# Kernel tuning notes

Measured on AMD Instinct MI355X. Metric: run time of the kernel, lower is better.

## Reference

```python
import jax, jax.numpy as jnp
import numpy as np

N_NODES = 100000
N_EDGES = 6400000
IN_CH, HID, OUT_CH = 14, 16, 8


def setup_inputs() -> dict:
    key = jax.random.key(0)
    ks = jax.random.split(key, 10)
    x = jax.random.normal(ks[0], (N_NODES, IN_CH), dtype=jnp.float32)
    edge_index = jax.random.randint(ks[1], (2, N_EDGES), 0, N_NODES, dtype=jnp.int64)
    edge_attr = jax.random.normal(ks[2], (N_EDGES, 4), dtype=jnp.float32)
    # SAGEConv params: lin_l (neighbor aggr, with bias), lin_r (root, no bias)
    def glorot(k, shape):
        fan_in = shape[1]
        return jax.random.normal(k, shape, dtype=jnp.float32) / jnp.sqrt(jnp.float32(fan_in))
    W1_l = glorot(ks[3], (HID, IN_CH)); b1 = jnp.zeros((HID,), jnp.float32)
    W1_r = glorot(ks[4], (HID, IN_CH))
    W2_l = glorot(ks[5], (OUT_CH, HID)); b2 = jnp.zeros((OUT_CH,), jnp.float32)
    W2_r = glorot(ks[6], (OUT_CH, HID))
    return {"x": x, "edge_index": edge_index, "edge_attr": edge_attr,
            "W1_l": W1_l, "b1": b1, "W1_r": W1_r,
            "W2_l": W2_l, "b2": b2, "W2_r": W2_r}


def sage_conv(x, src, dst, W_l, b_l, W_r):
    # mean aggregation of neighbor features at destination nodes
    msg = x[src]                                            # [E, F]
    s = jax.ops.segment_sum(msg, dst, num_segments=N_NODES)  # [N, F]
    cnt = jax.ops.segment_sum(jnp.ones((src.shape[0],), x.dtype), dst,
                              num_segments=N_NODES)
    mean = s / jnp.maximum(cnt, 1.0)[:, None]
    # out = lin_l(mean) + lin_r(x)
    return mean @ W_l.T + b_l + x @ W_r.T


def reference(x, edge_index, edge_attr, W1_l, b1, W1_r, W2_l, b2, W2_r):
    src, dst = edge_index[0], edge_index[1]
    h = jax.nn.relu(sage_conv(x, src, dst, W1_l, b1, W1_r))
    # F.dropout(training=self.training) -> identity in eval mode
    out = sage_conv(h, src, dst, W2_l, b2, W2_r)
    return out
```

## Files before the change

kernel.cpp:

```cpp
#include <hip/hip_runtime.h>

#define N_NODES 100000
#define N_EDGES 6400000
#define IN_CH 14
#define HID 16
#define OUT_CH 8

#define NBINS 1024
#define BINW 98
#define NCLS 8
#define SLABC 1152
#define BINREG (NCLS * SLABC)
#define BINBUF_WORDS (NBINS * BINREG)
#define SORT_CAP 7168
#define BF_THREADS 1024
#define BF_TILE 8192
#define BF_EPT (BF_TILE / BF_THREADS)
#define N_TILES ((N_EDGES + BF_TILE - 1) / BF_TILE)
#define LHN 128

__device__ __forceinline__ unsigned short f2bf(float f) {
    unsigned u = __float_as_uint(f);
    u += 0x7fffu + ((u >> 16) & 1u);
    return (unsigned short)(u >> 16);
}

__global__ void prep_kernel(const float* __restrict__ x, unsigned short* __restrict__ xb,
                            int* __restrict__ tail) {
    int i = blockIdx.x * blockDim.x + threadIdx.x;
    if (i < NCLS * NBINS) tail[i] = 0;
    if (i >= (NBINS * BINW) * 16) return;
    int n = i >> 4, c = i & 15;
    float v = (n < N_NODES && c < IN_CH) ? x[n * IN_CH + c] : 0.0f;
    xb[i] = f2bf(v);
}

__global__ __launch_bounds__(BF_THREADS)
void binfill_kernel(const uint4* __restrict__ src4, const uint4* __restrict__ dst4,
                    int* __restrict__ tail, unsigned* __restrict__ binbuf) {
    __shared__ unsigned stile[BF_TILE];
    __shared__ unsigned short stbin[BF_TILE];
    __shared__ int lh[NBINS];
    __shared__ int lx[NBINS];
    __shared__ int lofs[NBINS];
    __shared__ int wsum[16];

    const int t = threadIdx.x;
    const int lane = t & 63;
    const int wv = t >> 6;
    const int cls = blockIdx.x & (NCLS - 1);
    const long long tb = (long long)blockIdx.x * BF_TILE;

    lh[t] = 0;
    __syncthreads();

    unsigned epack[BF_EPT];
    int      ebin[BF_EPT];
    int      erank[BF_EPT];

#pragma unroll
    for (int sw = 0; sw < BF_EPT / 4; ++sw) {
        long long u = tb / 4 + (long long)sw * BF_THREADS + t;
        int k = sw * 4;
        if (u * 4 < N_EDGES) {
            uint4 s = src4[u];
            uint4 d = dst4[u];
            unsigned b;
            b = d.x / BINW; epack[k+0] = s.x | ((d.x - b*BINW) << 17); ebin[k+0] = (int)b; erank[k+0] = atomicAdd(&lh[b], 1);
            b = d.y / BINW; epack[k+1] = s.y | ((d.y - b*BINW) << 17); ebin[k+1] = (int)b; erank[k+1] = atomicAdd(&lh[b], 1);
            b = d.z / BINW; epack[k+2] = s.z | ((d.z - b*BINW) << 17); ebin[k+2] = (int)b; erank[k+2] = atomicAdd(&lh[b], 1);
            b = d.w / BINW; epack[k+3] = s.w | ((d.w - b*BINW) << 17); ebin[k+3] = (int)b; erank[k+3] = atomicAdd(&lh[b], 1);
        } else {
            ebin[k+0] = ebin[k+1] = ebin[k+2] = ebin[k+3] = -1;
        }
    }
    __syncthreads();

    int v = lh[t];
    int incl = v;
#pragma unroll
    for (int d = 1; d < 64; d <<= 1) {
        int o = __shfl_up(incl, d, 64);
        if (lane >= d) incl += o;
    }
    if (lane == 63) wsum[wv] = incl;
    __syncthreads();
    if (t < 16) {
        int s = wsum[t];
        int si = s;
#pragma unroll
        for (int d = 1; d < 16; d <<= 1) {
            int o = __shfl_up(si, d, 16);
            if (t >= d) si += o;
        }
        wsum[t] = si - s;
    }
    __syncthreads();
    lx[t] = incl - v + wsum[wv];
    lofs[t] = atomicAdd(&tail[cls * NBINS + t], v);
    __syncthreads();

#pragma unroll
    for (int k = 0; k < BF_EPT; ++k) {
        if (ebin[k] >= 0) {
            int pos = lx[ebin[k]] + erank[k];
            stile[pos] = epack[k];
            stbin[pos] = (unsigned short)ebin[k];
        }
    }
    __syncthreads();

    int cnt = (int)((N_EDGES - tb < BF_TILE) ? (N_EDGES - tb) : BF_TILE);
    for (int i = t; i < cnt; i += BF_THREADS) {
        int b = stbin[i];
        int slot = lofs[b] + (i - lx[b]);
        if ((unsigned)slot < (unsigned)SLABC)
            binbuf[b * BINREG + cls * SLABC + slot] = stile[i];
    }
}

__global__ __launch_bounds__(512)
void sortagg1_kernel(const unsigned* __restrict__ xb, const float* __restrict__ x,
                     unsigned* __restrict__ binbuf, const int* __restrict__ tail,
                     int* __restrict__ rowptr, int* __restrict__ deg,
                     const float* __restrict__ W_l, const float* __restrict__ bias,
                     const float* __restrict__ W_r,
                     float* __restrict__ h_f32, unsigned short* __restrict__ h_bf16) {
    __shared__ unsigned sbuf[SORT_CAP];
    __shared__ int lhist[LHN];
    __shared__ int loff[LHN];
    __shared__ int lcur[LHN];
    __shared__ int wtot[2];
    __shared__ int segcnt[NCLS];
    __shared__ int segoff[NCLS];
    __shared__ int totc[1];

    const int b = blockIdx.x;
    const int t = threadIdx.x;
    const int regbase = b * BINREG;

    if (t == 0) {
        int s = 0;
        for (int k = 0; k < NCLS; ++k) {
            int c = tail[k * NBINS + b];
            if (c < 0) c = 0;
            if (c > SLABC) c = SLABC;
            if (s + c > SORT_CAP) c = SORT_CAP - s;
            segcnt[k] = c; segoff[k] = s; s += c;
        }
        totc[0] = s;
    }
    if (t < LHN) lhist[t] = 0;
    __syncthreads();
    const int cnt = totc[0];

    for (int k = 0; k < NCLS; ++k) {
        const int base = regbase + k * SLABC;
        const int c = segcnt[k];
        for (int i = t; i < c; i += 512)
            atomicAdd(&lhist[binbuf[base + i] >> 17], 1);
    }
    __syncthreads();

    int v = (t < LHN) ? lhist[t] : 0;
    int incl = v;
#pragma unroll
    for (int d = 1; d < 64; d <<= 1) {
        int o = __shfl_up(incl, d, 64);
        if ((t & 63) >= d) incl += o;
    }
    if (t < LHN && (t & 63) == 63) wtot[t >> 6] = incl;
    __syncthreads();
    if (t < LHN) {
        int excl = incl - v + ((t >= 64) ? wtot[0] : 0);
        loff[t] = excl;
        lcur[t] = excl;
        if (t < BINW) {
            int gn = b * BINW + t;
            if (gn < N_NODES) { rowptr[gn] = regbase + excl; deg[gn] = v; }
        }
    }
    __syncthreads();

    for (int k = 0; k < NCLS; ++k) {
        const int base = regbase + k * SLABC;
        const int c = segcnt[k];
        for (int i = t; i < c; i += 512) {
            unsigned w = binbuf[base + i];
            unsigned ld = w >> 17;
            int pos = atomicAdd(&lcur[ld], 1);
            if (pos < cnt) sbuf[pos] = w & 0x1FFFFu;
        }
    }
    __syncthreads();

    for (int i = t; i < cnt; i += 512)
        binbuf[regbase + i] = sbuf[i];

    const int g = t >> 3;
    const int l = t & 7;
    float m0[2], m1[2];
#pragma unroll
    for (int p = 0; p < 2; ++p) {
        m0[p] = 0.0f; m1[p] = 0.0f;
        int n = g + 64 * p;
        if (n < BINW) {
            int dg = lhist[n];
            int off = loff[n];
            float a0 = 0.0f, a1 = 0.0f;
            int i = 0;
            for (; i + 4 <= dg; i += 4) {
                unsigned s0 = sbuf[off + i], s1 = sbuf[off + i + 1];
                unsigned s2 = sbuf[off + i + 2], s3 = sbuf[off + i + 3];
                unsigned u0 = xb[s0 * 8 + l];
                unsigned u1 = xb[s1 * 8 + l];
                unsigned u2 = xb[s2 * 8 + l];
                unsigned u3 = xb[s3 * 8 + l];
                a0 += __uint_as_float(u0 << 16);  a1 += __uint_as_float(u0 & 0xffff0000u);
                a0 += __uint_as_float(u1 << 16);  a1 += __uint_as_float(u1 & 0xffff0000u);
                a0 += __uint_as_float(u2 << 16);  a1 += __uint_as_float(u2 & 0xffff0000u);
                a0 += __uint_as_float(u3 << 16);  a1 += __uint_as_float(u3 & 0xffff0000u);
            }
            for (; i < dg; ++i) {
                unsigned u0 = xb[sbuf[off + i] * 8 + l];
                a0 += __uint_as_float(u0 << 16);  a1 += __uint_as_float(u0 & 0xffff0000u);
            }
            float inv = 1.0f / fmaxf((float)dg, 1.0f);
            m0[p] = a0 * inv; m1[p] = a1 * inv;
        }
    }
    __syncthreads();

    float* smean = (float*)sbuf;
#pragma unroll
    for (int p = 0; p < 2; ++p) {
        int n = g + 64 * p;
        if (n < BINW) {
            smean[n * 16 + 2 * l]     = m0[p];
            smean[n * 16 + 2 * l + 1] = m1[p];
        }
    }
    __syncthreads();

    const int nodeBase = b * BINW;
    for (int i = t; i < BINW * HID; i += 512) {
        int n = i >> 4, oc = i & 15;
        int gn = nodeBase + n;
        if (gn >= N_NODES) break;
        float a = bias[oc];
#pragma unroll
        for (int k = 0; k < IN_CH; ++k)
            a = fmaf(smean[n * 16 + k], W_l[oc * IN_CH + k],
                     fmaf(x[gn * IN_CH + k], W_r[oc * IN_CH + k], a));
        float vv = fmaxf(a, 0.0f);
        h_f32[gn * HID + oc] = vv;
        h_bf16[gn * HID + oc] = f2bf(vv);
    }
}

__global__ __launch_bounds__(256)
void agg2_kernel(const unsigned* __restrict__ hb,
                 const float* __restrict__ h_f32,
                 const unsigned* __restrict__ csr,
                 const int* __restrict__ rowptr, const int* __restrict__ deg,
                 const float* __restrict__ W_l, const float* __restrict__ bias,
                 const float* __restrict__ W_r, float* __restrict__ out) {
    __shared__ float smean[4][8][16];

    const int t = threadIdx.x;
    const int wv = t >> 6;
    const int lane = t & 63;
    const int g = lane >> 3;
    const int l = lane & 7;
    const int node = (blockIdx.x * 4 + wv) * 8 + g;

    int beg = rowptr[node];
    int d = deg[node];
    if (beg < 0) beg = 0;
    if (d < 0) d = 0;
    if (beg + d > BINBUF_WORDS) d = BINBUF_WORDS - beg;

    float a0 = 0.0f, a1 = 0.0f;
    int i = 0;
    for (; i + 8 <= d; i += 8) {
        unsigned s0 = csr[beg + i]     & 0x1FFFFu;
        unsigned s1 = csr[beg + i + 1] & 0x1FFFFu;
        unsigned s2 = csr[beg + i + 2] & 0x1FFFFu;
        unsigned s3 = csr[beg + i + 3] & 0x1FFFFu;
        unsigned s4 = csr[beg + i + 4] & 0x1FFFFu;
        unsigned s5 = csr[beg + i + 5] & 0x1FFFFu;
        unsigned s6 = csr[beg + i + 6] & 0x1FFFFu;
        unsigned s7 = csr[beg + i + 7] & 0x1FFFFu;
        unsigned u0 = hb[s0 * 8 + l];
        unsigned u1 = hb[s1 * 8 + l];
        unsigned u2 = hb[s2 * 8 + l];
        unsigned u3 = hb[s3 * 8 + l];
        unsigned u4 = hb[s4 * 8 + l];
        unsigned u5 = hb[s5 * 8 + l];
        unsigned u6 = hb[s6 * 8 + l];
        unsigned u7 = hb[s7 * 8 + l];
        a0 += __uint_as_float(u0 << 16);        a1 += __uint_as_float(u0 & 0xffff0000u);
        a0 += __uint_as_float(u1 << 16);        a1 += __uint_as_float(u1 & 0xffff0000u);
        a0 += __uint_as_float(u2 << 16);        a1 += __uint_as_float(u2 & 0xffff0000u);
        a0 += __uint_as_float(u3 << 16);        a1 += __uint_as_float(u3 & 0xffff0000u);
        a0 += __uint_as_float(u4 << 16);        a1 += __uint_as_float(u4 & 0xffff0000u);
        a0 += __uint_as_float(u5 << 16);        a1 += __uint_as_float(u5 & 0xffff0000u);
        a0 += __uint_as_float(u6 << 16);        a1 += __uint_as_float(u6 & 0xffff0000u);
        a0 += __uint_as_float(u7 << 16);        a1 += __uint_as_float(u7 & 0xffff0000u);
    }
    for (; i < d; ++i) {
        unsigned s0 = csr[beg + i] & 0x1FFFFu;
        unsigned u0 = hb[s0 * 8 + l];
        a0 += __uint_as_float(u0 << 16);        a1 += __uint_as_float(u0 & 0xffff0000u);
    }
    float inv = 1.0f / fmaxf((float)d, 1.0f);
    smean[wv][g][2 * l]     = a0 * inv;
    smean[wv][g][2 * l + 1] = a1 * inv;

    {
        int n8 = lane >> 3;
        int oc = lane & 7;
        int gn = (blockIdx.x * 4 + wv) * 8 + n8;
        float a = bias[oc];
#pragma unroll
        for (int k = 0; k < HID; ++k)
            a = fmaf(smean[wv][n8][k], W_l[oc * HID + k],
                     fmaf(h_f32[gn * HID + k], W_r[oc * HID + k], a));
        out[gn * OUT_CH + oc] = a;
    }
}

extern "C" void kernel_launch(void* const* d_in, const int* in_sizes, int n_in,
                              void* d_out, int out_size, void* d_ws, size_t ws_size,
                              hipStream_t stream) {
    const float* x    = (const float*)d_in[0];
    const int* eidx   = (const int*)d_in[1];
    const float* W1_l = (const float*)d_in[3];
    const float* b1   = (const float*)d_in[4];
    const float* W1_r = (const float*)d_in[5];
    const float* W2_l = (const float*)d_in[6];
    const float* b2   = (const float*)d_in[7];
    const float* W2_r = (const float*)d_in[8];
    float* out = (float*)d_out;

    const uint4* src4 = (const uint4*)eidx;
    const uint4* dst4 = (const uint4*)(eidx + N_EDGES);

    int*            wsi      = (int*)d_ws;
    unsigned*       binbuf   = (unsigned*)wsi;
    int*            tail     = wsi + 9437184;
    unsigned short* x_bf16   = (unsigned short*)(wsi + 9445376);
    unsigned short* h_bf16   = (unsigned short*)(wsi + 10248192);
    float*          h_f32    = (float*)(wsi + 11048192);
    int*            rowptr   = wsi + 12648192;
    int*            deg      = wsi + 12748544;

    prep_kernel<<<(NBINS * BINW * 16 + 1023) / 1024, 1024, 0, stream>>>(x, x_bf16, tail);
    binfill_kernel<<<N_TILES, BF_THREADS, 0, stream>>>(src4, dst4, tail, binbuf);
    sortagg1_kernel<<<NBINS, 512, 0, stream>>>((const unsigned*)x_bf16, x, binbuf, tail,
                                               rowptr, deg, W1_l, b1, W1_r, h_f32, h_bf16);
    agg2_kernel<<<3125, 256, 0, stream>>>((const unsigned*)h_bf16, h_f32, binbuf,
                                          rowptr, deg, W2_l, b2, W2_r, out);
}
```

Measured before the change: 294.7 us.

## Restructure layer-2 aggregation per bin with CSR staged in shared memory

The second-layer aggregation kernel now runs one 512-thread block per destination bin instead of 3125 blocks of 32 nodes. Each block loads the bin's sorted edge region into LDS with vectorized uint4 loads, then 8-lane groups gather bf16 neighbor features using source indices read from LDS. This replaces scattered per-node CSR loads from global memory with one coalesced bulk copy per bin. The cost is fewer blocks (1024), each handling two nodes per thread group, which lowers parallelism and latency hiding, and the unroll depth drops from 8 to 4.

```diff
diff --git a/kernel.cpp b/kernel.cpp
--- a/kernel.cpp
+++ b/kernel.cpp
@@ -18,6 +18,7 @@
 #define BF_EPT (BF_TILE / BF_THREADS)
 #define N_TILES ((N_EDGES + BF_TILE - 1) / BF_TILE)
 #define LHN 128
+
 
 __device__ __forceinline__ unsigned short f2bf(float f) {
     unsigned u = __float_as_uint(f);
@@ -258,73 +259,112 @@
     }
 }
 
-__global__ __launch_bounds__(256)
+__global__ __launch_bounds__(512)
 void agg2_kernel(const unsigned* __restrict__ hb,
                  const float* __restrict__ h_f32,
                  const unsigned* __restrict__ csr,
                  const int* __restrict__ rowptr, const int* __restrict__ deg,
                  const float* __restrict__ W_l, const float* __restrict__ bias,
                  const float* __restrict__ W_r, float* __restrict__ out) {
-    __shared__ float smean[4][8][16];
-
+    __shared__ __attribute__((aligned(16))) unsigned sbuf[SORT_CAP];
+    __shared__ int ldeg[LHN];
+    __shared__ int loff[LHN];
+    __shared__ int totc[1];
+
+    const int b = blockIdx.x;
     const int t = threadIdx.x;
-    const int wv = t >> 6;
-    const int lane = t & 63;
-    const int g = lane >> 3;
-    const int l = lane & 7;
-    const int node = (blockIdx.x * 4 + wv) * 8 + g;
-
-    int beg = rowptr[node];
-    int d = deg[node];
-    if (beg < 0) beg = 0;
-    if (d < 0) d = 0;
-    if (beg + d > BINBUF_WORDS) d = BINBUF_WORDS - beg;
-
-    float a0 = 0.0f, a1 = 0.0f;
-    int i = 0;
-    for (; i + 8 <= d; i += 8) {
-        unsigned s0 = csr[beg + i]     & 0x1FFFFu;
-        unsigned s1 = csr[beg + i + 1] & 0x1FFFFu;
-        unsigned s2 = csr[beg + i + 2] & 0x1FFFFu;
-        unsigned s3 = csr[beg + i + 3] & 0x1FFFFu;
-        unsigned s4 = csr[beg + i + 4] & 0x1FFFFu;
-        unsigned s5 = csr[beg + i + 5] & 0x1FFFFu;
-        unsigned s6 = csr[beg + i + 6] & 0x1FFFFu;
-        unsigned s7 = csr[beg + i + 7] & 0x1FFFFu;
-        unsigned u0 = hb[s0 * 8 + l];
-        unsigned u1 = hb[s1 * 8 + l];
-        unsigned u2 = hb[s2 * 8 + l];
-        unsigned u3 = hb[s3 * 8 + l];
-        unsigned u4 = hb[s4 * 8 + l];
-        unsigned u5 = hb[s5 * 8 + l];
-        unsigned u6 = hb[s6 * 8 + l];
-        unsigned u7 = hb[s7 * 8 + l];
-        a0 += __uint_as_float(u0 << 16);        a1 += __uint_as_float(u0 & 0xffff0000u);
-        a0 += __uint_as_float(u1 << 16);        a1 += __uint_as_float(u1 & 0xffff0000u);
-        a0 += __uint_as_float(u2 << 16);        a1 += __uint_as_float(u2 & 0xffff0000u);
-        a0 += __uint_as_float(u3 << 16);        a1 += __uint_as_float(u3 & 0xffff0000u);
-        a0 += __uint_as_float(u4 << 16);        a1 += __uint_as_float(u4 & 0xffff0000u);
-        a0 += __uint_as_float(u5 << 16);        a1 += __uint_as_float(u5 & 0xffff0000u);
-        a0 += __uint_as_float(u6 << 16);        a1 += __uint_as_float(u6 & 0xffff0000u);
-        a0 += __uint_as_float(u7 << 16);        a1 += __uint_as_float(u7 & 0xffff0000u);
-    }
-    for (; i < d; ++i) {
-        unsigned s0 = csr[beg + i] & 0x1FFFFu;
-        unsigned u0 = hb[s0 * 8 + l];
-        a0 += __uint_as_float(u0 << 16);        a1 += __uint_as_float(u0 & 0xffff0000u);
-    }
-    float inv = 1.0f / fmaxf((float)d, 1.0f);
-    smean[wv][g][2 * l]     = a0 * inv;
-    smean[wv][g][2 * l + 1] = a1 * inv;
+    const int regbase = b * BINREG;
+    const int nvalid = (N_NODES - b * BINW < BINW) ? (N_NODES - b * BINW) : BINW;
+
+    if (t < LHN) {
+        int gn = b * BINW + t;
+        int dv = 0, ov = 0;
+        if (t < BINW && gn < N_NODES) {
+            dv = deg[gn];
+            ov = rowptr[gn] - regbase;
+            if (dv < 0) dv = 0;
+            if (ov < 0) ov = 0;
+        }
+        ldeg[t] = dv;
+        loff[t] = ov;
+    }
+    if (t == 0) {
+        int last = nvalid - 1;
+        int c = (last >= 0) ? (rowptr[b * BINW + last] - regbase + deg[b * BINW + last]) : 0;
+        if (c < 0) c = 0;
+        if (c > SORT_CAP) c = SORT_CAP;
+        totc[0] = c;
+    }
+    __syncthreads();
+    const int cnt = totc[0];
 
     {
-        int n8 = lane >> 3;
-        int oc = lane & 7;
-        int gn = (blockIdx.x * 4 + wv) * 8 + n8;
+        const uint4* c4 = (const uint4*)(csr + regbase);
+        uint4* s4 = (uint4*)sbuf;
+        const int nv = cnt >> 2;
+        for (int i = t; i < nv; i += 512) s4[i] = c4[i];
+        int r = (nv << 2) + t;
+        if (r < cnt) sbuf[r] = csr[regbase + r];
+    }
+    __syncthreads();
+
+    const int g = t >> 3;
+    const int l = t & 7;
+    float m0[2], m1[2];
+#pragma unroll
+    for (int p = 0; p < 2; ++p) {
+        m0[p] = 0.0f; m1[p] = 0.0f;
+        int n = g + 64 * p;
+        if (n < BINW) {
+            int dg = ldeg[n];
+            int off = loff[n];
+            if (off + dg > cnt) dg = (cnt > off) ? (cnt - off) : 0;
+            float a0 = 0.0f, a1 = 0.0f;
+            int i = 0;
+            for (; i + 4 <= dg; i += 4) {
+                unsigned s0 = sbuf[off + i]     & 0x1FFFFu;
+                unsigned s1 = sbuf[off + i + 1] & 0x1FFFFu;
+                unsigned s2 = sbuf[off + i + 2] & 0x1FFFFu;
+                unsigned s3 = sbuf[off + i + 3] & 0x1FFFFu;
+                unsigned u0 = hb[s0 * 8 + l];
+                unsigned u1 = hb[s1 * 8 + l];
+                unsigned u2 = hb[s2 * 8 + l];
+                unsigned u3 = hb[s3 * 8 + l];
+                a0 += __uint_as_float(u0 << 16);  a1 += __uint_as_float(u0 & 0xffff0000u);
+                a0 += __uint_as_float(u1 << 16);  a1 += __uint_as_float(u1 & 0xffff0000u);
+                a0 += __uint_as_float(u2 << 16);  a1 += __uint_as_float(u2 & 0xffff0000u);
+                a0 += __uint_as_float(u3 << 16);  a1 += __uint_as_float(u3 & 0xffff0000u);
+            }
+            for (; i < dg; ++i) {
+                unsigned u0 = hb[(sbuf[off + i] & 0x1FFFFu) * 8 + l];
+                a0 += __uint_as_float(u0 << 16);  a1 += __uint_as_float(u0 & 0xffff0000u);
+            }
+            float inv = 1.0f / fmaxf((float)dg, 1.0f);
+            m0[p] = a0 * inv; m1[p] = a1 * inv;
+        }
+    }
+    __syncthreads();
+
+    float* smean = (float*)sbuf;
+#pragma unroll
+    for (int p = 0; p < 2; ++p) {
+        int n = g + 64 * p;
+        if (n < BINW) {
+            smean[n * 16 + 2 * l]     = m0[p];
+            smean[n * 16 + 2 * l + 1] = m1[p];
+        }
+    }
+    __syncthreads();
+
+    const int nodeBase = b * BINW;
+    for (int i = t; i < BINW * OUT_CH; i += 512) {
+        int n = i >> 3, oc = i & 7;
+        int gn = nodeBase + n;
+        if (gn >= N_NODES) break;
         float a = bias[oc];
 #pragma unroll
         for (int k = 0; k < HID; ++k)
-            a = fmaf(smean[wv][n8][k], W_l[oc * HID + k],
+            a = fmaf(smean[n * 16 + k], W_l[oc * HID + k],
                      fmaf(h_f32[gn * HID + k], W_r[oc * HID + k], a));
         out[gn * OUT_CH + oc] = a;
     }
@@ -359,6 +399,6 @@
     binfill_kernel<<<N_TILES, BF_THREADS, 0, stream>>>(src4, dst4, tail, binbuf);
     sortagg1_kernel<<<NBINS, 512, 0, stream>>>((const unsigned*)x_bf16, x, binbuf, tail,
                                                rowptr, deg, W1_l, b1, W1_r, h_f32, h_bf16);
-    agg2_kernel<<<3125, 256, 0, stream>>>((const unsigned*)h_bf16, h_f32, binbuf,
-                                          rowptr, deg, W2_l, b2, W2_r, out);
-}
+    agg2_kernel<<<NBINS, 512, 0, stream>>>((const unsigned*)h_bf16, h_f32, binbuf,
+                                           rowptr, deg, W2_l, b2, W2_r, out);
+}
```

Measured after the change: 286.9 us. -2.6%, faster.
